# Kernel optimization log

Hardware: AMD Instinct MI355X
Metric: run time of the kernel (lower is better)

The kernel has to match this reference:

```python
import jax, jax.numpy as jnp
import numpy as np

B, T, F, U, P = 64, 4096, 128, 128, 16  # batch, timesteps, filters, units, skip


def setup_inputs() -> dict:
    key = jax.random.key(0)
    k1, k2, k3, k4 = jax.random.split(key, 4)
    inputs = jax.random.normal(k1, (B, T, F), dtype=jnp.float32)
    # Keras GRUCell params (reset_after=True, default): kernel [F,3U],
    # recurrent_kernel [U,3U], bias [2,3U] (input bias + recurrent bias).
    kernel = jax.random.normal(k2, (F, 3 * U), dtype=jnp.float32) * (1.0 / np.sqrt(F))
    recurrent_kernel = jax.random.normal(k3, (U, 3 * U), dtype=jnp.float32) * (1.0 / np.sqrt(U))
    bias = jax.random.normal(k4, (2, 3 * U), dtype=jnp.float32) * 0.01
    return {"inputs": inputs, "kernel": kernel,
            "recurrent_kernel": recurrent_kernel, "bias": bias}


def reference(inputs, kernel, recurrent_kernel, bias):
    # SkipGRU: h[t] = GRUCell(x[t], h[t-P]) with h[t]=GRUCell(x[t], 0) for t<P.
    # This factorizes into P independent GRU chains of length T//P, which we
    # fold into the batch axis and run with one lax.scan.
    Bs, Ts, Fs = inputs.shape
    Us = recurrent_kernel.shape[0]
    Ls = Ts // P  # chain length
    # [B,T,F] -> [B,L,P,F] -> [B,P,L,F] -> [B*P,L,F]; chain j holds steps t=l*P+j
    x = inputs.reshape(Bs, Ls, P, Fs).transpose(0, 2, 1, 3).reshape(Bs * P, Ls, Fs)
    b_in, b_rec = bias[0], bias[1]
    # Precompute input projections for all steps: [B*P, L, 3U]
    xm = jnp.einsum('blf,fu->blu', x, kernel) + b_in

    def step(h, xt):
        hm = h @ recurrent_kernel + b_rec              # [B*P, 3U]
        z = jax.nn.sigmoid(xt[:, :Us] + hm[:, :Us])
        r = jax.nn.sigmoid(xt[:, Us:2 * Us] + hm[:, Us:2 * Us])
        hh = jax.nn.relu(xt[:, 2 * Us:] + r * hm[:, 2 * Us:])  # activation='relu'
        h_new = z * h + (1.0 - z) * hh
        return h_new, h_new

    h0 = jnp.zeros((Bs * P, Us), dtype=inputs.dtype)
    _, outs = jax.lax.scan(step, h0, xm.transpose(1, 0, 2))  # outs: [L, B*P, U]
    # [L,B*P,U] -> [B,P,L,U] -> [B,L,P,U] -> [B,T,U] (return_sequences=True)
    outs = outs.transpose(1, 0, 2).reshape(Bs, P, Ls, Us)
    outs = outs.transpose(0, 2, 1, 3).reshape(Bs, Ts, Us)
    return outs
```

## Files before the change

kernel.cpp:

```cpp
#include <hip/hip_runtime.h>
#include <hip/hip_bf16.h>


#define B_N 64
#define T_N 4096
#define F_N 128
#define U_N 128
#define P_N 16
#define L_N 256
#define NW 8
#define NT (NW * 64)

typedef _Float16 f16x8 __attribute__((ext_vector_type(8)));
typedef _Float16 f16x4 __attribute__((ext_vector_type(4)));
typedef float f32x4 __attribute__((ext_vector_type(4)));

__device__ __forceinline__ float sigmoidf_(float x) {
    return __builtin_amdgcn_rcpf(1.0f + __expf(-x));
}

__device__ __forceinline__ int fpos(int k) {
    return ((k >> 5) << 5) + (((k >> 2) & 3) << 3) + (((k >> 4) & 1) << 2) + (k & 3);
}

#define BAR() do { \
    asm volatile("s_waitcnt lgkmcnt(0)" ::: "memory"); \
    __builtin_amdgcn_s_barrier(); \
    __builtin_amdgcn_sched_barrier(0); \
} while (0)

struct Acc { f32x4 z, r, xh, hh; };

__global__ __launch_bounds__(NT, 2) void skipgru_kernel(
    const float* __restrict__ xg, const float* __restrict__ Wk,
    const float* __restrict__ Wr, const float* __restrict__ bias,
    float* __restrict__ out)
{
    __shared__ __align__(16) _Float16 A_x[2][16][132];
    __shared__ __align__(16) _Float16 A_h[2][16][132];

    const int tid  = threadIdx.x;
    const int lane = tid & 63;
    const int wave = tid >> 6;
    const int ln   = lane & 15;
    const int lg   = lane >> 4;
    const int u    = wave * 16 + ln;
    const int m0   = lg * 4;
    const int b    = blockIdx.x;
    const int hcol = fpos(u);

    const float bz  = bias[u]       + bias[384 + u];
    const float br  = bias[128 + u] + bias[384 + 128 + u];
    const float bxh = bias[256 + u];
    const float brh = bias[384 + 256 + u];

    f16x8 wzk[4], wzr[4], wrk[4], wrr[4], whk[4], whr[4];
    #pragma unroll
    for (int kt = 0; kt < 4; ++kt) {
        #pragma unroll
        for (int e = 0; e < 8; ++e) {
            int k = kt * 32 + ((e >> 2) << 4) + (lg << 2) + (e & 3);
            const float* wkp = Wk + (size_t)k * 384;
            const float* wrp = Wr + (size_t)k * 384;
            wzk[kt][e] = (_Float16)wkp[u];
            wzr[kt][e] = (_Float16)wrp[u];
            wrk[kt][e] = (_Float16)wkp[128 + u];
            wrr[kt][e] = (_Float16)wrp[128 + u];
            whk[kt][e] = (_Float16)wkp[256 + u];
            whr[kt][e] = (_Float16)wrp[256 + u];
        }
    }

    for (int q = tid; q < 16 * 132; q += NT) ((_Float16*)A_h[0])[q] = (_Float16)0;

    const int sm = tid & 15, sc = (tid >> 4) << 2;
    const int scp = fpos(sc);
    const float* xb = xg + (size_t)b * T_N * F_N;
    {
        float4 x0 = *(const float4*)(xb + (size_t)sm * F_N + sc);
        float4 x1 = *(const float4*)(xb + (size_t)(P_N + sm) * F_N + sc);
        f16x4 v0 = {(_Float16)x0.x, (_Float16)x0.y, (_Float16)x0.z, (_Float16)x0.w};
        f16x4 v1 = {(_Float16)x1.x, (_Float16)x1.y, (_Float16)x1.z, (_Float16)x1.w};
        *(f16x4*)&A_x[0][sm][scp] = v0;
        *(f16x4*)&A_x[1][sm][scp] = v1;
    }
    float4 xsB = *(const float4*)(xb + (size_t)(2 * P_N + sm) * F_N + sc);
    float4 xsA = *(const float4*)(xb + (size_t)(3 * P_N + sm) * F_N + sc);

    f32x4 hreg = {0.f, 0.f, 0.f, 0.f};
    float* op = out + ((size_t)b * T_N + m0) * U_N + u;
    __syncthreads();

    Acc P, Q;
    {
        f16x8 axf[4];
        #pragma unroll
        for (int kt = 0; kt < 4; ++kt)
            axf[kt] = *(const f16x8*)&A_x[0][ln][kt * 32 + lg * 8];
        P.z  = {bz, bz, bz, bz};
        P.r  = {br, br, br, br};
        P.xh = {bxh, bxh, bxh, bxh};
        P.hh = {brh, brh, brh, brh};
        #pragma unroll
        for (int kt = 0; kt < 4; ++kt) {
            P.z  = __builtin_amdgcn_mfma_f32_16x16x32_f16(axf[kt], wzk[kt], P.z, 0, 0, 0);
            P.r  = __builtin_amdgcn_mfma_f32_16x16x32_f16(axf[kt], wrk[kt], P.r, 0, 0, 0);
            P.xh = __builtin_amdgcn_mfma_f32_16x16x32_f16(axf[kt], whk[kt], P.xh, 0, 0, 0);
        }
    }

    auto step = [&](int l, float4& xs, Acc& cur, Acc& nxt) {
        const int rbuf = l & 1, wbuf = (l + 1) & 1;
        f16x8 ahf[4];
        #pragma unroll
        for (int kt = 0; kt < 4; ++kt)
            ahf[kt] = *(const f16x8*)&A_h[rbuf][ln][kt * 32 + lg * 8];
        #pragma unroll
        for (int kt = 0; kt < 4; ++kt) {
            cur.z  = __builtin_amdgcn_mfma_f32_16x16x32_f16(ahf[kt], wzr[kt], cur.z, 0, 0, 0);
            cur.r  = __builtin_amdgcn_mfma_f32_16x16x32_f16(ahf[kt], wrr[kt], cur.r, 0, 0, 0);
            cur.hh = __builtin_amdgcn_mfma_f32_16x16x32_f16(ahf[kt], whr[kt], cur.hh, 0, 0, 0);
        }
        if (l + 1 < L_N) {
            f16x8 axf[4];
            #pragma unroll
            for (int kt = 0; kt < 4; ++kt)
                axf[kt] = *(const f16x8*)&A_x[wbuf][ln][kt * 32 + lg * 8];
            nxt.z  = {bz, bz, bz, bz};
            nxt.r  = {br, br, br, br};
            nxt.xh = {bxh, bxh, bxh, bxh};
            nxt.hh = {brh, brh, brh, brh};
            #pragma unroll
            for (int kt = 0; kt < 4; ++kt) {
                nxt.z  = __builtin_amdgcn_mfma_f32_16x16x32_f16(axf[kt], wzk[kt], nxt.z, 0, 0, 0);
                nxt.r  = __builtin_amdgcn_mfma_f32_16x16x32_f16(axf[kt], wrk[kt], nxt.r, 0, 0, 0);
                nxt.xh = __builtin_amdgcn_mfma_f32_16x16x32_f16(axf[kt], whk[kt], nxt.xh, 0, 0, 0);
            }
        }
        #pragma unroll
        for (int e = 0; e < 4; ++e) {
            float z = sigmoidf_(cur.z[e]);
            float r = sigmoidf_(cur.r[e]);
            float c = fmaxf(0.f, fmaf(r, cur.hh[e], cur.xh[e]));
            float hn = fmaf(z, hreg[e] - c, c);
            hreg[e] = hn;
            A_h[wbuf][m0 + e][hcol] = (_Float16)hn;
            op[(size_t)e * U_N] = hn;
        }
        op += P_N * U_N;
        if (l + 2 < L_N) {
            f16x4 v = {(_Float16)xs.x, (_Float16)xs.y, (_Float16)xs.z, (_Float16)xs.w};
            *(f16x4*)&A_x[rbuf][sm][scp] = v;
            if (l + 4 < L_N)
                xs = *(const float4*)(xb + (size_t)((l + 4) * P_N + sm) * F_N + sc);
        }
        BAR();
    };

    for (int l = 0; l < L_N; l += 2) {
        step(l, xsB, P, Q);
        step(l + 1, xsA, Q, P);
    }
}

extern "C" void kernel_launch(void* const* d_in, const int* in_sizes, int n_in,
                              void* d_out, int out_size, void* d_ws, size_t ws_size,
                              hipStream_t stream) {
    const float* inputs = (const float*)d_in[0];
    const float* kernel = (const float*)d_in[1];
    const float* rker   = (const float*)d_in[2];
    const float* bias   = (const float*)d_in[3];
    float* o = (float*)d_out;
    hipLaunchKernelGGL(skipgru_kernel, dim3(B_N), dim3(NT), 0, stream,
                       inputs, kernel, rker, bias, o);
}
```

Before: 186.5 us.

## Split GRU into parallel input-projection GEMM and recurrent-only scan kernel

```diff
diff --git a/kernel.cpp b/kernel.cpp
--- a/kernel.cpp
+++ b/kernel.cpp
@@ -11,6 +11,12 @@
 #define NW 8
 #define NT (NW * 64)
 
+#define XM_BYTES  (64ULL * 4096 * 384 * 2)
+#define WKF_OFF   XM_BYTES
+#define WKF_ELEMS (24 * 4 * 64 * 8)
+#define BC_OFF    (WKF_OFF + (size_t)WKF_ELEMS * 2)
+#define WS_NEED   (BC_OFF + 384 * 4)
+
 typedef _Float16 f16x8 __attribute__((ext_vector_type(8)));
 typedef _Float16 f16x4 __attribute__((ext_vector_type(4)));
 typedef float f32x4 __attribute__((ext_vector_type(4)));
@@ -29,9 +35,158 @@
     __builtin_amdgcn_sched_barrier(0); \
 } while (0)
 
+__global__ void prep_kernel(const float* __restrict__ Wk,
+                            const float* __restrict__ bias,
+                            _Float16* __restrict__ wkf,
+                            float* __restrict__ bc)
+{
+    int q = blockIdx.x * 256 + threadIdx.x;
+    if (q < WKF_ELEMS) {
+        int e = q & 7, lane = (q >> 3) & 63, kt = (q >> 9) & 3, n = q >> 11;
+        int lg = lane >> 4, ln = lane & 15;
+        int k = kt * 32 + ((e >> 2) << 4) + (lg << 2) + (e & 3);
+        wkf[q] = (_Float16)Wk[(size_t)k * 384 + n * 16 + ln];
+    }
+    if (q < 384)
+        bc[q] = bias[q] + (q < 256 ? bias[384 + q] : 0.0f);
+}
+
+__global__ __launch_bounds__(256, 1) void phase1_kernel(
+    const float* __restrict__ xg, const _Float16* __restrict__ wkf,
+    const float* __restrict__ bc, _Float16* __restrict__ xm)
+{
+    __shared__ __align__(16) _Float16 A[128][132];
+    __shared__ __align__(16) _Float16 BF[WKF_ELEMS];
+
+    const int tid = threadIdx.x, lane = tid & 63, wave = tid >> 6;
+    const int ln = lane & 15, lg = lane >> 4;
+    const size_t row0 = (size_t)blockIdx.x * 128;
+
+    for (int q = tid; q < WKF_ELEMS / 4; q += 256)
+        ((ushort4*)BF)[q] = ((const ushort4*)wkf)[q];
+    for (int q = tid; q < 4096; q += 256) {
+        int r = q >> 5, c = (q & 31) << 2;
+        float4 v = *(const float4*)(xg + (row0 + r) * F_N + c);
+        f16x4 h = {(_Float16)v.x, (_Float16)v.y, (_Float16)v.z, (_Float16)v.w};
+        *(f16x4*)&A[r][fpos(c)] = h;
+    }
+    __syncthreads();
+
+    f16x8 af[2][4];
+    #pragma unroll
+    for (int i = 0; i < 2; ++i)
+        #pragma unroll
+        for (int kt = 0; kt < 4; ++kt)
+            af[i][kt] = *(const f16x8*)&A[(2 * wave + i) * 16 + ln][kt * 32 + lg * 8];
+
+    for (int n = 0; n < 24; ++n) {
+        f16x8 bf[4];
+        #pragma unroll
+        for (int kt = 0; kt < 4; ++kt)
+            bf[kt] = *(const f16x8*)&BF[(((n * 4 + kt) * 64 + lane) << 3)];
+        float bcn = bc[n * 16 + ln];
+        #pragma unroll
+        for (int i = 0; i < 2; ++i) {
+            f32x4 acc = {bcn, bcn, bcn, bcn};
+            #pragma unroll
+            for (int kt = 0; kt < 4; ++kt)
+                acc = __builtin_amdgcn_mfma_f32_16x16x32_f16(af[i][kt], bf[kt], acc, 0, 0, 0);
+            _Float16* op = xm + (row0 + (2 * wave + i) * 16 + lg * 4) * 384 + n * 16 + ln;
+            #pragma unroll
+            for (int e = 0; e < 4; ++e) op[(size_t)e * 384] = (_Float16)acc[e];
+        }
+    }
+}
+
+struct XmSet { _Float16 z0,z1,z2,z3, r0,r1,r2,r3, h0,h1,h2,h3; };
+#define LOAD_XM(S, l) do { const _Float16* _p = xmlane + (size_t)(l) * 6144; \
+    S.z0=_p[0];   S.z1=_p[384];  S.z2=_p[768];  S.z3=_p[1152]; \
+    S.r0=_p[128]; S.r1=_p[512];  S.r2=_p[896];  S.r3=_p[1280]; \
+    S.h0=_p[256]; S.h1=_p[640];  S.h2=_p[1024]; S.h3=_p[1408]; } while (0)
+
+__global__ __launch_bounds__(NT, 2) void phase2_kernel(
+    const float* __restrict__ Wr, const float* __restrict__ bias,
+    const _Float16* __restrict__ xm, float* __restrict__ out)
+{
+    __shared__ __align__(16) _Float16 A_h[2][16][132];
+
+    const int tid  = threadIdx.x;
+    const int lane = tid & 63;
+    const int wave = tid >> 6;
+    const int ln   = lane & 15;
+    const int lg   = lane >> 4;
+    const int u    = wave * 16 + ln;
+    const int m0   = lg * 4;
+    const int b    = blockIdx.x;
+    const int hcol = fpos(u);
+
+    const float brh = bias[384 + 256 + u];
+
+    f16x8 wzr[4], wrr[4], whr[4];
+    #pragma unroll
+    for (int kt = 0; kt < 4; ++kt) {
+        #pragma unroll
+        for (int e = 0; e < 8; ++e) {
+            int k = kt * 32 + ((e >> 2) << 4) + (lg << 2) + (e & 3);
+            const float* wrp = Wr + (size_t)k * 384;
+            wzr[kt][e] = (_Float16)wrp[u];
+            wrr[kt][e] = (_Float16)wrp[128 + u];
+            whr[kt][e] = (_Float16)wrp[256 + u];
+        }
+    }
+
+    for (int q = tid; q < 16 * 132; q += NT) ((_Float16*)A_h[0])[q] = (_Float16)0;
+
+    const _Float16* xmlane = xm + ((size_t)b * T_N + m0) * 384 + u;
+    XmSet SA, SB;
+    LOAD_XM(SA, 0);
+    LOAD_XM(SB, 1);
+
+    f32x4 hreg = {0.f, 0.f, 0.f, 0.f};
+    float* op = out + ((size_t)b * T_N + m0) * U_N + u;
+    __syncthreads();
+
+    auto step = [&](int l, XmSet& S) {
+        const int rbuf = l & 1, wbuf = (l + 1) & 1;
+        f16x8 ahf[4];
+        #pragma unroll
+        for (int kt = 0; kt < 4; ++kt)
+            ahf[kt] = *(const f16x8*)&A_h[rbuf][ln][kt * 32 + lg * 8];
+        f32x4 az  = {(float)S.z0, (float)S.z1, (float)S.z2, (float)S.z3};
+        f32x4 ar  = {(float)S.r0, (float)S.r1, (float)S.r2, (float)S.r3};
+        f32x4 ahh = {brh, brh, brh, brh};
+        float xh0 = (float)S.h0, xh1 = (float)S.h1, xh2 = (float)S.h2, xh3 = (float)S.h3;
+        #pragma unroll
+        for (int kt = 0; kt < 4; ++kt) {
+            az  = __builtin_amdgcn_mfma_f32_16x16x32_f16(ahf[kt], wzr[kt], az, 0, 0, 0);
+            ar  = __builtin_amdgcn_mfma_f32_16x16x32_f16(ahf[kt], wrr[kt], ar, 0, 0, 0);
+            ahh = __builtin_amdgcn_mfma_f32_16x16x32_f16(ahf[kt], whr[kt], ahh, 0, 0, 0);
+        }
+        if (l + 2 < L_N) LOAD_XM(S, l + 2);
+        float xh[4] = {xh0, xh1, xh2, xh3};
+        #pragma unroll
+        for (int e = 0; e < 4; ++e) {
+            float z = sigmoidf_(az[e]);
+            float r = sigmoidf_(ar[e]);
+            float c = fmaxf(0.f, fmaf(r, ahh[e], xh[e]));
+            float hn = fmaf(z, hreg[e] - c, c);
+            hreg[e] = hn;
+            A_h[wbuf][m0 + e][hcol] = (_Float16)hn;
+            op[(size_t)e * U_N] = hn;
+        }
+        op += P_N * U_N;
+        BAR();
+    };
+
+    for (int l = 0; l < L_N; l += 2) {
+        step(l, SA);
+        step(l + 1, SB);
+    }
+}
+
 struct Acc { f32x4 z, r, xh, hh; };
 
-__global__ __launch_bounds__(NT, 2) void skipgru_kernel(
+__global__ __launch_bounds__(NT, 2) void skipgru_mono(
     const float* __restrict__ xg, const float* __restrict__ Wk,
     const float* __restrict__ Wr, const float* __restrict__ bias,
     float* __restrict__ out)
@@ -171,6 +326,19 @@
     const float* rker   = (const float*)d_in[2];
     const float* bias   = (const float*)d_in[3];
     float* o = (float*)d_out;
-    hipLaunchKernelGGL(skipgru_kernel, dim3(B_N), dim3(NT), 0, stream,
-                       inputs, kernel, rker, bias, o);
-}
+
+    if (ws_size >= WS_NEED) {
+        _Float16* xm  = (_Float16*)d_ws;
+        _Float16* wkf = (_Float16*)((char*)d_ws + WKF_OFF);
+        float*    bc  = (float*)((char*)d_ws + BC_OFF);
+        hipLaunchKernelGGL(prep_kernel, dim3(192), dim3(256), 0, stream,
+                           kernel, bias, wkf, bc);
+        hipLaunchKernelGGL(phase1_kernel, dim3(2048), dim3(256), 0, stream,
+                           inputs, wkf, bc, xm);
+        hipLaunchKernelGGL(phase2_kernel, dim3(B_N), dim3(NT), 0, stream,
+                           rker, bias, xm, o);
+    } else {
+        hipLaunchKernelGGL(skipgru_mono, dim3(B_N), dim3(NT), 0, stream,
+                           inputs, kernel, rker, bias, o);
+    }
+}
```

Result: slower. 424.2 us (+127.4%).
